# Kernel tuning notes

Hardware: AMD Instinct MI355X
Metric: run time of the kernel (lower is better)

Reference implementation:

```python
import jax, jax.numpy as jnp
import numpy as np

SEQ = 4096
NUM_INP = 1024
NUM_OUT = 128
NUM_HEADS = 8
NUM_HIDDEN = 64  # hardcoded in __init__
LN_EPS = 1e-5


def setup_inputs() -> dict:
    key = jax.random.key(0)
    ks = jax.random.split(key, 7)
    d_kq = NUM_HEADS * NUM_HIDDEN
    d_v = NUM_HEADS * NUM_OUT
    lim = 1.0 / np.sqrt(NUM_INP)
    return {
        "x": jax.random.normal(ks[0], (SEQ, NUM_INP), dtype=jnp.float32),
        "Wk": jax.random.uniform(ks[1], (d_kq, NUM_INP), jnp.float32, -lim, lim),
        "bk": jax.random.uniform(ks[2], (d_kq,), jnp.float32, -lim, lim),
        "Wq": jax.random.uniform(ks[3], (d_kq, NUM_INP), jnp.float32, -lim, lim),
        "bq": jax.random.uniform(ks[4], (d_kq,), jnp.float32, -lim, lim),
        "Wv": jax.random.uniform(ks[5], (d_v, NUM_INP), jnp.float32, -lim, lim),
        "bv": jax.random.uniform(ks[6], (d_v,), jnp.float32, -lim, lim),
        "ln_w": jnp.ones((NUM_OUT,), jnp.float32),
        "ln_b": jnp.zeros((NUM_OUT,), jnp.float32),
    }


def reference(x, Wk, bk, Wq, bq, Wv, bv, ln_w, ln_b):
    S = x.shape[0]
    # projections (eqx.nn.Linear: y = W @ x + b)
    k = (x @ Wk.T + bk).reshape(S, NUM_HEADS, NUM_HIDDEN)
    k = k / jnp.sqrt(jnp.asarray(NUM_HIDDEN, k.dtype))
    q = (x @ Wq.T + bq).reshape(S, NUM_HEADS, NUM_HIDDEN)
    v = (x @ Wv.T + bv).reshape(S, NUM_HEADS, NUM_OUT)
    # logits[i, j, h] = sum_k keys[i,h,k] * queries[j,h,k]
    logits = jnp.einsum('ihk,jhk->ijh', k, q)
    # softmax over axis=1 (the j / query axis, as in the original)
    attn = jax.nn.softmax(logits, axis=1)
    # contract over j AND heads -> [S, NUM_OUT]
    out = jnp.einsum('ijh,jhe->ie', attn, v)
    # LayerNorm over last dim with affine params
    mu = jnp.mean(out, axis=-1, keepdims=True)
    var = jnp.var(out, axis=-1, keepdims=True)
    normed = (out - mu) / jnp.sqrt(var + LN_EPS)
    return normed * ln_w + ln_b
```

## Files before the change

kernel.cpp:

```cpp
#include <hip/hip_runtime.h>
#include <hip/hip_bf16.h>

#define SEQ   4096
#define NINP  1024
#define NH    8
#define ND    64
#define NE    128
#define DKQ   512
#define DV    1024

typedef __attribute__((ext_vector_type(8))) short  short8;
typedef __attribute__((ext_vector_type(4))) float  floatx4;
typedef __attribute__((ext_vector_type(4))) unsigned short ushortx4;

__device__ __forceinline__ unsigned short f2bf(float f) {
    union { float f; unsigned int i; } v; v.f = f;
    unsigned int r = v.i + 0x7fffu + ((v.i >> 16) & 1u);
    return (unsigned short)(r >> 16);
}
__device__ __forceinline__ unsigned int pkperm(float hi, float lo) {
    return __builtin_amdgcn_perm(__float_as_uint(hi), __float_as_uint(lo), 0x07060302u);
}
__device__ __forceinline__ short8 pk8p(float4 a, float4 b) {
    int4 w;
    w.x = (int)pkperm(a.y, a.x);
    w.y = (int)pkperm(a.w, a.z);
    w.z = (int)pkperm(b.y, b.x);
    w.w = (int)pkperm(b.w, b.z);
    return *(short8*)&w;
}
__device__ __forceinline__ floatx4 mfma16(short8 a, short8 b, floatx4 c) {
    return __builtin_amdgcn_mfma_f32_16x16x32_bf16(a, b, c, 0, 0, 0);
}
__device__ __forceinline__ void gload_lds16(const unsigned short* g, unsigned short* l) {
    __builtin_amdgcn_global_load_lds(
        (const __attribute__((address_space(1))) unsigned int*)g,
        (__attribute__((address_space(3))) unsigned int*)l, 16, 0, 0);
}

__global__ __launch_bounds__(256)
void conv_kernel(const float* __restrict__ x,  const float* __restrict__ Wk,
                 const float* __restrict__ Wq, const float* __restrict__ Wv,
                 unsigned short* __restrict__ xbf,  unsigned short* __restrict__ Wkbf,
                 unsigned short* __restrict__ Wqbf, unsigned short* __restrict__ Wvbf)
{
    size_t idx = (size_t)blockIdx.x * 256 + threadIdx.x;
    const float* src; unsigned short* dst; size_t off;
    if      (idx < 524288)  { src = x;  dst = xbf;  off = idx; }
    else if (idx < 589824)  { src = Wk; dst = Wkbf; off = idx - 524288; }
    else if (idx < 655360)  { src = Wq; dst = Wqbf; off = idx - 589824; }
    else                    { src = Wv; dst = Wvbf; off = idx - 655360; }
    float4 a = *(const float4*)(src + off * 8);
    float4 b = *(const float4*)(src + off * 8 + 4);
    *(short8*)(dst + off * 8) = pk8p(a, b);
}

__global__ __launch_bounds__(256, 4)
void proj_kernel(const unsigned short* __restrict__ xbf,
                 const unsigned short* __restrict__ Wkbf, const float* __restrict__ bk,
                 const unsigned short* __restrict__ Wqbf, const float* __restrict__ bq,
                 const unsigned short* __restrict__ Wvbf, const float* __restrict__ bvv,
                 unsigned short* __restrict__ Kbuf, unsigned short* __restrict__ Qfrag,
                 unsigned short* __restrict__ Vfrag)
{
    __shared__ unsigned short As[128][64];
    __shared__ unsigned short Bs[64][64];

    const int ct = blockIdx.x;
    const int m0 = blockIdx.y * 128;

    const unsigned short* W; const float* bias;
    int colbase; float scale; int dest;
    if (ct < 8)       { W = Wkbf; bias = bk;  colbase = ct * 64;        scale = 0.18033688f; dest = 0; }
    else if (ct < 16) { W = Wqbf; bias = bq;  colbase = (ct - 8) * 64;  scale = 1.0f;        dest = 1; }
    else              { W = Wvbf; bias = bvv; colbase = (ct - 16) * 64; scale = 1.0f;        dest = 2; }

    const int tid  = threadIdx.x;
    const int wv   = tid >> 6;
    const int lane = tid & 63;
    const int n    = lane & 15;
    const int qd   = lane >> 4;
    const int wr   = wv >> 1, wc = wv & 1;

    const int l8 = lane >> 3, l7 = lane & 7;
    const unsigned short* pA = xbf + (size_t)(m0 + l8) * NINP + (l7 ^ l8) * 8;
    const unsigned short* pB = W  + (size_t)(colbase + l8) * NINP + (l7 ^ l8) * 8;

    floatx4 acc[4][2] = {};

    for (int k0 = 0; k0 < NINP; k0 += 64) {
        #pragma unroll
        for (int t = 0; t < 4; ++t)
            gload_lds16(pA + (size_t)(wv*32 + t*8) * NINP + k0, &As[wv*32 + t*8][0]);
        #pragma unroll
        for (int t = 0; t < 2; ++t)
            gload_lds16(pB + (size_t)(wv*16 + t*8) * NINP + k0, &Bs[wv*16 + t*8][0]);
        __syncthreads();
        #pragma unroll
        for (int kk = 0; kk < 2; ++kk) {
            short8 af[4], bf2[2];
            #pragma unroll
            for (int mi = 0; mi < 4; ++mi) {
                const int R = wr*64 + mi*16 + n;
                af[mi] = *(const short8*)&As[R][((kk*4 + qd) ^ (R & 7)) * 8];
            }
            #pragma unroll
            for (int ni = 0; ni < 2; ++ni) {
                const int R = wc*32 + ni*16 + n;
                bf2[ni] = *(const short8*)&Bs[R][((kk*4 + qd) ^ (R & 7)) * 8];
            }
            #pragma unroll
            for (int mi = 0; mi < 4; ++mi)
                #pragma unroll
                for (int ni = 0; ni < 2; ++ni)
                    acc[mi][ni] = mfma16(af[mi], bf2[ni], acc[mi][ni]);
        }
        __syncthreads();
    }

    #pragma unroll
    for (int mi = 0; mi < 4; ++mi) {
        #pragma unroll
        for (int ni = 0; ni < 2; ++ni) {
            int o = colbase + wc*32 + ni*16 + n;
            float bfv = bias[o];
            int srow = m0 + wr*64 + mi*16 + qd*4;
            if (dest == 2) {
                int hh = o >> 7, e = o & 127;
                int e16 = e >> 4, ne = e & 15;
                int jt = srow >> 5, qd_a = (srow >> 3) & 3, t0 = srow & 7;
                ushortx4 pkv;
                #pragma unroll
                for (int r = 0; r < 4; ++r) pkv[r] = f2bf(acc[mi][ni][r] + bfv);
                *(ushortx4*)(Vfrag + (((size_t)hh*128 + jt)*8 + e16)*512
                             + (qd_a*16 + ne)*8 + t0) = pkv;
            } else if (dest == 1) {
                int hh = o >> 6, d = o & 63;
                int dd = d >> 5, qd_l = (d >> 3) & 3, t = d & 7;
                int jt = srow >> 5, a = (srow >> 4) & 1;
                size_t base = (((size_t)hh*128 + jt)*4 + (a + 2*dd))*512 + t;
                #pragma unroll
                for (int r = 0; r < 4; ++r) {
                    int nl = (srow + r) & 15;
                    Qfrag[base + (qd_l*16 + nl)*8] = f2bf(acc[mi][ni][r] + bfv);
                }
            } else {
                #pragma unroll
                for (int r = 0; r < 4; ++r)
                    Kbuf[(size_t)(srow + r) * DKQ + o] = f2bf((acc[mi][ni][r] + bfv) * scale);
            }
        }
    }
}

__global__ __launch_bounds__(256, 2)
void attn_kernel(const unsigned short* __restrict__ Kbuf,
                 const unsigned short* __restrict__ Qfrag,
                 const unsigned short* __restrict__ Vfrag,
                 float* __restrict__ Obuf,
                 float* dout)
{
    __shared__ unsigned char smem[35840];
    float* Red0 = (float*)smem;
    float* Red1 = Red0 + 64 * 68;
    float* DenS = Red1 + 64 * 68;

    const int b    = blockIdx.x;
    const int h    = b & 7;
    const int i0   = (b >> 3) * 64;
    const int tid  = threadIdx.x;
    const int j_q  = tid >> 6;
    const int lane = tid & 63;
    const int n    = lane & 15;
    const int qd   = lane >> 4;

    short8 kf[4][2];
    #pragma unroll
    for (int g = 0; g < 4; ++g)
        #pragma unroll
        for (int d = 0; d < 2; ++d)
            kf[g][d] = *(const short8*)(Kbuf + (size_t)(i0 + g*16 + n) * DKQ
                                        + h * ND + d*32 + qd*8);

    floatx4 acc[8][4] = {};
    float den[4] = {0.f, 0.f, 0.f, 0.f};

    const int adA = (((qd & 1) << 5) + n) * 4;
    const int adB = adA + 64;
    const bool lo = (qd < 2);

    const unsigned short* Qbase = Qfrag + (size_t)h * 128 * 4 * 512 + lane * 8;
    const unsigned short* Vbase = Vfrag + (size_t)h * 128 * 8 * 512 + lane * 8;

    for (int k = 0; k < 32; ++k) {
        const int jt = j_q * 32 + k;

        const unsigned short* Qb = Qbase + (size_t)jt * 2048;
        short8 qf00 = *(const short8*)(Qb);
        short8 qf10 = *(const short8*)(Qb + 512);
        short8 qf01 = *(const short8*)(Qb + 1024);
        short8 qf11 = *(const short8*)(Qb + 1536);
        const unsigned short* Vb = Vbase + (size_t)jt * 4096;
        short8 vf[8];
        #pragma unroll
        for (int e16 = 0; e16 < 8; ++e16)
            vf[e16] = *(const short8*)(Vb + e16 * 512);

        #pragma unroll
        for (int gc = 0; gc < 2; ++gc) {
            floatx4 s[2][2] = {};
            #pragma unroll
            for (int gi = 0; gi < 2; ++gi) {
                const int g = gc*2 + gi;
                s[0][gi] = mfma16(qf00, kf[g][0], s[0][gi]); s[0][gi] = mfma16(qf01, kf[g][1], s[0][gi]);
                s[1][gi] = mfma16(qf10, kf[g][0], s[1][gi]); s[1][gi] = mfma16(qf11, kf[g][1], s[1][gi]);
            }

            int pkk[2][2][2];
            #pragma unroll
            for (int a = 0; a < 2; ++a)
                #pragma unroll
                for (int gi = 0; gi < 2; ++gi) {
                    float p0 = __builtin_amdgcn_exp2f(s[a][gi][0]);
                    float p1 = __builtin_amdgcn_exp2f(s[a][gi][1]);
                    float p2 = __builtin_amdgcn_exp2f(s[a][gi][2]);
                    float p3 = __builtin_amdgcn_exp2f(s[a][gi][3]);
                    den[gc*2 + gi] += (p0 + p1) + (p2 + p3);
                    pkk[a][gi][0] = (int)pkperm(p1, p0);
                    pkk[a][gi][1] = (int)pkperm(p3, p2);
                }

            short8 bfrag[2];
            #pragma unroll
            for (int gi = 0; gi < 2; ++gi) {
                int w0a = __builtin_amdgcn_ds_bpermute(adA, pkk[0][gi][0]);
                int w1a = __builtin_amdgcn_ds_bpermute(adA, pkk[0][gi][1]);
                int w2a = __builtin_amdgcn_ds_bpermute(adB, pkk[0][gi][0]);
                int w3a = __builtin_amdgcn_ds_bpermute(adB, pkk[0][gi][1]);
                int w0b = __builtin_amdgcn_ds_bpermute(adA, pkk[1][gi][0]);
                int w1b = __builtin_amdgcn_ds_bpermute(adA, pkk[1][gi][1]);
                int w2b = __builtin_amdgcn_ds_bpermute(adB, pkk[1][gi][0]);
                int w3b = __builtin_amdgcn_ds_bpermute(adB, pkk[1][gi][1]);
                int4 wv4;
                wv4.x = lo ? w0a : w0b;
                wv4.y = lo ? w1a : w1b;
                wv4.z = lo ? w2a : w2b;
                wv4.w = lo ? w3a : w3b;
                bfrag[gi] = *(short8*)&wv4;
            }

            #pragma unroll
            for (int e16 = 0; e16 < 8; ++e16) {
                acc[e16][gc*2]     = mfma16(vf[e16], bfrag[0], acc[e16][gc*2]);
                acc[e16][gc*2 + 1] = mfma16(vf[e16], bfrag[1], acc[e16][gc*2 + 1]);
            }
        }
    }

    #pragma unroll
    for (int g = 0; g < 4; ++g) {
        den[g] += __shfl_xor(den[g], 16);
        den[g] += __shfl_xor(den[g], 32);
    }
    if (lane < 16) {
        #pragma unroll
        for (int g = 0; g < 4; ++g)
            DenS[j_q*64 + g*16 + lane] = den[g];
    }

    #pragma unroll
    for (int eh = 0; eh < 2; ++eh) {
        if (eh) __syncthreads();
        if (j_q >= 2) {
            float* Rb = (j_q == 2) ? Red0 : Red1;
            #pragma unroll
            for (int e = 0; e < 4; ++e)
                #pragma unroll
                for (int g = 0; g < 4; ++g)
                    *(floatx4*)&Rb[(g*16 + n)*68 + e*16 + qd*4] = acc[eh*4 + e][g];
        }
        __syncthreads();
        if (j_q == 1) {
            #pragma unroll
            for (int e = 0; e < 4; ++e)
                #pragma unroll
                for (int g = 0; g < 4; ++g) {
                    float* p = &Red1[(g*16 + n)*68 + e*16 + qd*4];
                    floatx4 o = *(const floatx4*)p;
                    floatx4 r = acc[eh*4 + e][g];
                    r[0] += o[0]; r[1] += o[1]; r[2] += o[2]; r[3] += o[3];
                    *(floatx4*)p = r;
                }
        } else if (j_q == 0) {
            #pragma unroll
            for (int e = 0; e < 4; ++e)
                #pragma unroll
                for (int g = 0; g < 4; ++g) {
                    floatx4 o = *(const floatx4*)&Red0[(g*16 + n)*68 + e*16 + qd*4];
                    acc[eh*4 + e][g][0] += o[0]; acc[eh*4 + e][g][1] += o[1];
                    acc[eh*4 + e][g][2] += o[2]; acc[eh*4 + e][g][3] += o[3];
                }
        }
        __syncthreads();
        if (j_q == 0) {
            #pragma unroll
            for (int e = 0; e < 4; ++e)
                #pragma unroll
                for (int g = 0; g < 4; ++g) {
                    floatx4 o = *(const floatx4*)&Red1[(g*16 + n)*68 + e*16 + qd*4];
                    floatx4 r = acc[eh*4 + e][g];
                    r[0] += o[0]; r[1] += o[1]; r[2] += o[2]; r[3] += o[3];
                    float* dst = Obuf + ((size_t)h * SEQ + i0 + g*16 + n) * NE
                                 + (eh*4 + e)*16 + qd*4;
                    *(floatx4*)dst = r;
                }
        }
    }

    if (j_q == 0) {
        dout[(size_t)(i0 + lane) * NE + h] =
            DenS[lane] + DenS[64 + lane] + DenS[128 + lane] + DenS[192 + lane];
    }
}

__global__ __launch_bounds__(256)
void ln_kernel(const float* __restrict__ Obuf,
               const float* __restrict__ lnA,
               const float* __restrict__ lnB,
               float* out)
{
    const bool aIsW = (lnA[0] == 1.0f);
    const float* lw = aIsW ? lnA : lnB;
    const float* lb = aIsW ? lnB : lnA;

    const int i    = blockIdx.x * 4 + (threadIdx.x >> 6);
    const int lane = threadIdx.x & 63;
    const int e0   = lane * 2;

    float inv[8];
    #pragma unroll
    for (int h = 0; h < 8; ++h) inv[h] = 1.0f / out[(size_t)i * NE + h];

    float x0 = 0.f, x1 = 0.f;
    #pragma unroll
    for (int h = 0; h < 8; ++h) {
        const float* p = Obuf + ((size_t)h * SEQ + i) * NE + e0;
        x0 += p[0] * inv[h]; x1 += p[1] * inv[h];
    }
    float s = x0 + x1, s2 = x0*x0 + x1*x1;
    #pragma unroll
    for (int off = 1; off < 64; off <<= 1) {
        s  += __shfl_xor(s,  off);
        s2 += __shfl_xor(s2, off);
    }
    float mu   = s * (1.f / 128.f);
    float var  = s2 * (1.f / 128.f) - mu * mu;
    float rstd = rsqrtf(var + 1e-5f);
    float2 y;
    y.x = (x0 - mu) * rstd * lw[e0]     + lb[e0];
    y.y = (x1 - mu) * rstd * lw[e0 + 1] + lb[e0 + 1];
    *(float2*)(out + (size_t)i * NE + e0) = y;
}

extern "C" void kernel_launch(void* const* d_in, const int* in_sizes, int n_in,
                              void* d_out, int out_size, void* d_ws, size_t ws_size,
                              hipStream_t stream)
{
    long long smax = 0;
    for (int i = 0; i < n_in; ++i) if ((long long)in_sizes[i] > smax) smax = in_sizes[i];
    const float *x = nullptr, *Wk = nullptr, *Wq = nullptr, *Wv = nullptr;
    const float *bk = nullptr, *bq = nullptr, *bv = nullptr, *lnA = nullptr, *lnB = nullptr;
    for (int i = 0; i < n_in; ++i) {
        long long s = in_sizes[i];
        const float* p = (const float*)d_in[i];
        if      (s == smax)          { x = p; }
        else if (s * 4 == smax)      { Wv = p; }
        else if (s * 8 == smax)      { if (!Wk) Wk = p; else Wq = p; }
        else if (s * 4096 == smax)   { bv = p; }
        else if (s * 8192 == smax)   { if (!bk) bk = p; else bq = p; }
        else if (s * 32768 == smax)  { if (!lnA) lnA = p; else lnB = p; }
    }

    unsigned short* Kbuf  = (unsigned short*)d_ws;
    unsigned short* Qfrag = Kbuf + (size_t)SEQ * DKQ;
    unsigned short* Vfrag = Qfrag + (size_t)SEQ * DKQ;
    unsigned short* xbf   = Vfrag + (size_t)NH * NE * SEQ;
    unsigned short* Wkbf  = xbf + (size_t)SEQ * NINP;
    unsigned short* Wqbf  = Wkbf + (size_t)DKQ * NINP;
    unsigned short* Wvbf  = Wqbf + (size_t)DKQ * NINP;
    float*          Obuf  = (float*)xbf;
    float*          out   = (float*)d_out;

    conv_kernel<<<dim3(3072), 256, 0, stream>>>(x, Wk, Wq, Wv, xbf, Wkbf, Wqbf, Wvbf);
    proj_kernel<<<dim3(32, 32), 256, 0, stream>>>(xbf, Wkbf, bk, Wqbf, bq, Wvbf, bv,
                                                  Kbuf, Qfrag, Vfrag);
    attn_kernel<<<dim3(512), 256, 0, stream>>>(Kbuf, Qfrag, Vfrag, Obuf, out);
    ln_kernel<<<dim3(1024), 256, 0, stream>>>(Obuf, lnA, lnB, out);
}
```

Baseline: 169.1 us.

## Stage Q/V fragments through LDS with async global-to-LDS prefetch

Replaces direct per-iteration global loads of Q and V fragments in the attention loop with async global-to-LDS loads. Q is double-buffered and V single-buffered per wave, with explicit vmcnt waits so the next tile's loads overlap the current MFMA work. LDS grows to 64KB, which may cap blocks per CU below the launch-bounds target of 2. The hand-tuned waitcnt counts and the single V buffer add ordering risk, and the last iteration prefetches one tile beyond the wave's range.

```diff
diff --git a/kernel.cpp b/kernel.cpp
--- a/kernel.cpp
+++ b/kernel.cpp
@@ -160,10 +160,10 @@
                  float* __restrict__ Obuf,
                  float* dout)
 {
-    __shared__ unsigned char smem[35840];
+    __shared__ unsigned char smem[65536];
     float* Red0 = (float*)smem;
-    float* Red1 = Red0 + 64 * 68;
-    float* DenS = Red1 + 64 * 68;
+    float* Red1 = (float*)(smem + 17408);
+    float* DenS = (float*)(smem + 34816);
 
     const int b    = blockIdx.x;
     const int h    = b & 7;
@@ -174,6 +174,9 @@
     const int n    = lane & 15;
     const int qd   = lane >> 4;
 
+    unsigned short* Qlds = (unsigned short*)smem + j_q * 4096;
+    unsigned short* Vlds = (unsigned short*)smem + 16384 + j_q * 4096;
+
     short8 kf[4][2];
     #pragma unroll
     for (int g = 0; g < 4; ++g)
@@ -191,21 +194,33 @@
 
     const unsigned short* Qbase = Qfrag + (size_t)h * 128 * 4 * 512 + lane * 8;
     const unsigned short* Vbase = Vfrag + (size_t)h * 128 * 8 * 512 + lane * 8;
-
+    const int jt0 = j_q * 32;
+
+    {
+        const unsigned short* qsrc = Qbase + (size_t)jt0 * 2048;
+        #pragma unroll
+        for (int c = 0; c < 4; ++c) gload_lds16(qsrc + c*512, Qlds + c*512);
+        const unsigned short* vsrc = Vbase + (size_t)jt0 * 4096;
+        #pragma unroll
+        for (int c = 0; c < 8; ++c) gload_lds16(vsrc + c*512, Vlds + c*512);
+    }
+
+    int cur = 0;
     for (int k = 0; k < 32; ++k) {
-        const int jt = j_q * 32 + k;
-
-        const unsigned short* Qb = Qbase + (size_t)jt * 2048;
-        short8 qf00 = *(const short8*)(Qb);
-        short8 qf10 = *(const short8*)(Qb + 512);
-        short8 qf01 = *(const short8*)(Qb + 1024);
-        short8 qf11 = *(const short8*)(Qb + 1536);
-        const unsigned short* Vb = Vbase + (size_t)jt * 4096;
-        short8 vf[8];
-        #pragma unroll
-        for (int e16 = 0; e16 < 8; ++e16)
-            vf[e16] = *(const short8*)(Vb + e16 * 512);
-
+        asm volatile("s_waitcnt vmcnt(8)" ::: "memory");
+        const unsigned short* Qc = Qlds + cur*2048 + lane*8;
+        short8 qf00 = *(const short8*)(Qc);
+        short8 qf10 = *(const short8*)(Qc + 512);
+        short8 qf01 = *(const short8*)(Qc + 1024);
+        short8 qf11 = *(const short8*)(Qc + 1536);
+        {
+            const unsigned short* qsrc = Qbase + (size_t)(jt0 + k + 1) * 2048;
+            unsigned short* qdst = Qlds + (cur ^ 1) * 2048;
+            #pragma unroll
+            for (int c = 0; c < 4; ++c) gload_lds16(qsrc + c*512, qdst + c*512);
+        }
+
+        short8 bfragA[2][2];
         #pragma unroll
         for (int gc = 0; gc < 2; ++gc) {
             floatx4 s[2][2] = {};
@@ -215,7 +230,6 @@
                 s[0][gi] = mfma16(qf00, kf[g][0], s[0][gi]); s[0][gi] = mfma16(qf01, kf[g][1], s[0][gi]);
                 s[1][gi] = mfma16(qf10, kf[g][0], s[1][gi]); s[1][gi] = mfma16(qf11, kf[g][1], s[1][gi]);
             }
-
             int pkk[2][2][2];
             #pragma unroll
             for (int a = 0; a < 2; ++a)
@@ -229,8 +243,6 @@
                     pkk[a][gi][0] = (int)pkperm(p1, p0);
                     pkk[a][gi][1] = (int)pkperm(p3, p2);
                 }
-
-            short8 bfrag[2];
             #pragma unroll
             for (int gi = 0; gi < 2; ++gi) {
                 int w0a = __builtin_amdgcn_ds_bpermute(adA, pkk[0][gi][0]);
@@ -246,16 +258,33 @@
                 wv4.y = lo ? w1a : w1b;
                 wv4.z = lo ? w2a : w2b;
                 wv4.w = lo ? w3a : w3b;
-                bfrag[gi] = *(short8*)&wv4;
+                bfragA[gc][gi] = *(short8*)&wv4;
             }
-
-            #pragma unroll
-            for (int e16 = 0; e16 < 8; ++e16) {
-                acc[e16][gc*2]     = mfma16(vf[e16], bfrag[0], acc[e16][gc*2]);
-                acc[e16][gc*2 + 1] = mfma16(vf[e16], bfrag[1], acc[e16][gc*2 + 1]);
-            }
-        }
-    }
+        }
+
+        asm volatile("s_waitcnt vmcnt(4)" ::: "memory");
+        short8 vf[8];
+        #pragma unroll
+        for (int e16 = 0; e16 < 8; ++e16)
+            vf[e16] = *(const short8*)(Vlds + e16*512 + lane*8);
+
+        #pragma unroll
+        for (int e16 = 0; e16 < 8; ++e16) {
+            acc[e16][0] = mfma16(vf[e16], bfragA[0][0], acc[e16][0]);
+            acc[e16][1] = mfma16(vf[e16], bfragA[0][1], acc[e16][1]);
+            acc[e16][2] = mfma16(vf[e16], bfragA[1][0], acc[e16][2]);
+            acc[e16][3] = mfma16(vf[e16], bfragA[1][1], acc[e16][3]);
+        }
+        __builtin_amdgcn_sched_barrier(0);
+        {
+            const unsigned short* vsrc = Vbase + (size_t)(jt0 + k + 1) * 4096;
+            #pragma unroll
+            for (int c = 0; c < 8; ++c) gload_lds16(vsrc + c*512, Vlds + c*512);
+        }
+        cur ^= 1;
+    }
+
+    __syncthreads();
 
     #pragma unroll
     for (int g = 0; g < 4; ++g) {
```

New measurement: 181.2 us. 7.1% more time.
